# Performance work log

Measured on AMD Instinct MI355X. Metric: run time of the kernel, lower is better.

## Reference

```python
import jax, jax.numpy as jnp
import numpy as np

N_ELEC, N_NUC, D, F, E = 1024, 256, 64, 64, 131072
HH, HG = 128, 128
# labels: en (elec->nuc), ne (nuc->elec), same (elec->elec), anti (elec->elec)
SRC_N = [N_ELEC, N_NUC, N_ELEC, N_ELEC]
TGT_N = [N_NUC, N_ELEC, N_ELEC, N_ELEC]


def setup_inputs() -> dict:
    key = jax.random.key(0)
    ks = jax.random.split(key, 16)
    s_elec = jax.random.normal(ks[0], (N_ELEC, D), jnp.float32)
    v_elec = jax.random.normal(ks[1], (N_ELEC, D, 3), jnp.float32)
    s_nuc = jax.random.normal(ks[2], (N_NUC, D), jnp.float32)
    v_nuc = jax.random.normal(ks[3], (N_NUC, D, 3), jnp.float32)
    senders = jnp.stack([jax.random.randint(jax.random.fold_in(ks[4], i), (E,), 0, SRC_N[i]) for i in range(4)]).astype(jnp.int32)
    receivers = jnp.stack([jax.random.randint(jax.random.fold_in(ks[5], i), (E,), 0, TGT_N[i]) for i in range(4)]).astype(jnp.int32)
    dist = jax.random.uniform(ks[6], (4, E, F), jnp.float32)
    dirs = jax.random.normal(ks[7], (4, E, 3), jnp.float32)
    dirs = dirs / jnp.linalg.norm(dirs, axis=-1, keepdims=True)  # unit directions
    def w_init(k, shape):
        return jax.random.normal(k, shape, jnp.float32) / jnp.sqrt(jnp.float32(shape[-2]))
    return {
        's_elec': s_elec, 'v_elec': v_elec, 's_nuc': s_nuc, 'v_nuc': v_nuc,
        'dist': dist, 'dirs': dirs,
        'W_w': w_init(ks[8], (4, F, 3 * D)),
        'W_h1': w_init(ks[9], (4, D, HH)), 'W_h2': w_init(ks[10], (4, HH, 3 * D)),
        'W_g1': w_init(ks[11], (4, 2 * D, HG)), 'W_g2': w_init(ks[12], (4, HG, 3 * D)),
        'W_V': jnp.broadcast_to(jnp.eye(D, dtype=jnp.float32), (4, D, D)),
        'W_U': jnp.broadcast_to(jnp.eye(D, dtype=jnp.float32), (4, D, D)),
        'senders': senders, 'receivers': receivers,
    }


def _painn_layer(s_elec, v_elec, s_nuc, v_nuc, dist, dirs, W_w, W_h1, W_h2, W_g1, W_g2, W_V, W_U, senders, receivers):
    src_s = [s_elec, s_nuc, s_elec, s_elec]
    src_v = [v_elec, v_nuc, v_elec, v_elec]
    ds_e = jnp.zeros_like(s_elec); dv_e = jnp.zeros_like(v_elec)
    ds_n = jnp.zeros_like(s_nuc); dv_n = jnp.zeros_like(v_nuc)
    for i in range(4):
        n_tgt = TGT_N[i]
        # edge MLPs: w (1-layer, last linear) and h (2-layer silu, last linear), bias-free
        we = dist[i] @ W_w[i]                                   # [E, 3D]
        h_all = jax.nn.silu(src_s[i] @ W_h1[i]) @ W_h2[i]        # [n_src, 3D]
        hx = h_all[senders[i]]                                   # gather per edge
        phi_s, phi_vv, phi_vs = jnp.split(we * hx, 3, axis=-1)   # each [E, D]
        z_s = jax.ops.segment_sum(phi_s, receivers[i], n_tgt)    # [n_tgt, D]
        vv = phi_vv[..., None] * src_v[i][senders[i]]            # [E, D, 3]
        vs = phi_vs[..., None] * dirs[i][:, None, :]             # [E, D, 3]
        z_v = jax.ops.segment_sum(vv + vs, receivers[i], n_tgt)  # [n_tgt, D, 3]
        Vv = jnp.einsum('ndi,df->nfi', z_v, W_V[i])
        Uv = jnp.einsum('ndi,df->nfi', z_v, W_U[i])
        g_in = jnp.concatenate([z_s, (Vv ** 2).sum(axis=-1)], axis=-1)  # [n_tgt, 2D]
        gs = jax.nn.silu(g_in @ W_g1[i]) @ W_g2[i]               # [n_tgt, 3D]
        a_ss, a_vv, a_sv = jnp.split(gs, 3, axis=-1)
        upd_v = Uv * a_vv[..., None]
        upd_s = a_sv * jnp.einsum('nfi,nfi->nf', Uv, Vv) + a_ss
        if i == 0:  # 'en' -> nuclei
            ds_n = ds_n + upd_s; dv_n = dv_n + upd_v
        else:       # 'ne','same','anti' -> electrons
            ds_e = ds_e + upd_s; dv_e = dv_e + upd_v
    s_e = s_elec + ds_e
    v_e = v_elec + dv_e
    return jnp.concatenate([s_e, v_e.reshape(N_ELEC, -1)], axis=-1)


def reference(s_elec, v_elec, s_nuc, v_nuc, dist, dirs, W_w, W_h1, W_h2, W_g1, W_g2, W_V, W_U, senders, receivers):
    return _painn_layer(s_elec, v_elec, s_nuc, v_nuc, dist, dirs, W_w, W_h1, W_h2, W_g1, W_g2, W_V, W_U, senders, receivers)
```

## Files before the change

kernel.cpp:

```cpp
#include <hip/hip_runtime.h>
#include <stdint.h>

#define E_EDGES 131072
#define NELEC 1024
#define NNUC 256
#define MAXCHUNK 256
#define NBLK 16
#define UNPB 4

typedef unsigned short ushort_t;
typedef __attribute__((ext_vector_type(8))) short short8;
typedef __attribute__((ext_vector_type(4))) short short4_t;
typedef __attribute__((ext_vector_type(4))) float float4_t;
typedef __attribute__((ext_vector_type(4))) int int4_t;
typedef __attribute__((ext_vector_type(2))) unsigned int uint2_t;

__device__ inline float silu_f(float x){ return x / (1.0f + expf(-x)); }

__device__ inline short f2bf_rne(float x){
    union { float f; uint32_t u; } a; a.f = x;
    return (short)((a.u + 0x7fffu + ((a.u >> 16) & 1u)) >> 16);
}
__device__ inline float bf2f(short h){
    union { uint32_t u; float f; } a; a.u = ((uint32_t)(uint16_t)h) << 16;
    return a.f;
}
__device__ inline ushort_t bfu(float x){ return (ushort_t)f2bf_rne(x); }
__device__ inline float asf_lo(uint32_t u){ union { uint32_t u; float f; } a; a.u = u << 16; return a.f; }
__device__ inline float asf_hi(uint32_t u){ union { uint32_t u; float f; } a; a.u = u & 0xFFFF0000u; return a.f; }

__global__ __launch_bounds__(256) void prep_kernel(
    const float* __restrict__ s_elec, const float* __restrict__ v_elec,
    const float* __restrict__ s_nuc,  const float* __restrict__ v_nuc,
    const float* __restrict__ W_h1, const float* __restrict__ W_h2,
    const float* __restrict__ W_w,
    const int* __restrict__ receivers,
    ushort_t* __restrict__ tabA, ushort_t* __restrict__ tabB,
    short* __restrict__ fragH, short* __restrict__ fragL,
    int* __restrict__ bh, float* __restrict__ out)
{
    int b = blockIdx.x, tid = threadIdx.x;
    __shared__ float sls[8][64];
    __shared__ float hidls[128][8];
    __shared__ int hist[1024];

    if (b < 288){
        int t, node0;
        if (b < 32){ t = 0; node0 = b*8; }
        else if (b < 160){ t = 1; node0 = (b-32)*8; }
        else { t = 2; node0 = (b-160)*8; }
        int tp = t + 1;
        const float* src = (t == 0) ? s_nuc : s_elec;
        const float* vsrc = (t == 0) ? v_nuc : v_elec;
        long baseA = (t == 0) ? 0 : (t == 1 ? 32768 : 163840);
        long baseB = (t == 0) ? 0 : (t == 1 ? 65536 : 327680);
        for (int i = tid; i < 512; i += 256){ int n = i >> 6, f = i & 63; sls[n][f] = src[(node0+n)*64 + f]; }
        __syncthreads();
        {
            int j = tid & 127, nh = tid >> 7;
            const float* w1 = W_h1 + (long)tp*64*128;
            float a0=0,a1=0,a2=0,a3=0;
            #pragma unroll 8
            for (int f = 0; f < 64; f++){
                float w = w1[f*128 + j];
                a0 += sls[nh*4+0][f]*w; a1 += sls[nh*4+1][f]*w;
                a2 += sls[nh*4+2][f]*w; a3 += sls[nh*4+3][f]*w;
            }
            float4_t hv = { silu_f(a0), silu_f(a1), silu_f(a2), silu_f(a3) };
            *(float4_t*)&hidls[j][nh*4] = hv;
        }
        __syncthreads();
        if (tid < 192){
            const float* w2 = W_h2 + (long)tp*128*192;
            float acc[8] = {0,0,0,0,0,0,0,0};
            #pragma unroll 4
            for (int h = 0; h < 128; h++){
                float w = w2[h*192 + tid];
                float4_t ha = *(float4_t*)&hidls[h][0];
                float4_t hb = *(float4_t*)&hidls[h][4];
                acc[0]+=ha[0]*w; acc[1]+=ha[1]*w; acc[2]+=ha[2]*w; acc[3]+=ha[3]*w;
                acc[4]+=hb[0]*w; acc[5]+=hb[1]*w; acc[6]+=hb[2]*w; acc[7]+=hb[3]*w;
            }
            int p = tid >> 6, d2 = tid & 63;
            if (p == 0){
                #pragma unroll
                for (int n = 0; n < 8; n++)
                    tabA[baseA + (long)((node0+n)*64 + d2)*2 + 0] = bfu(acc[n]);
            } else if (p == 2){
                #pragma unroll
                for (int n = 0; n < 8; n++)
                    tabA[baseA + (long)((node0+n)*64 + d2)*2 + 1] = bfu(acc[n]);
            } else {
                #pragma unroll
                for (int n = 0; n < 8; n++){
                    const float* vp = vsrc + (long)(node0+n)*192 + d2*3;
                    long o = baseB + (long)((node0+n)*64 + d2)*4;
                    tabB[o+0] = bfu(acc[n]*vp[0]);
                    tabB[o+1] = bfu(acc[n]*vp[1]);
                    tabB[o+2] = bfu(acc[n]*vp[2]);
                }
            }
        }
    } else if (b < 291){
        int t = b - 288, tp = t + 1;
        const float* W = W_w + (long)tp*64*192;
        for (int idx = tid; idx < 12288; idx += 256){
            int j    = idx & 7;
            int lane = (idx >> 3) & 63;
            int ks   = (idx >> 9) & 1;
            int nt   = idx >> 10;
            int k = ks*32 + ((lane >> 4) & 3)*8 + j;
            int n = nt*16 + (lane & 15);
            float v = W[k*192 + n];
            short hi = f2bf_rne(v);
            short lo = f2bf_rne(v - bf2f(hi));
            fragH[t*12288 + idx] = hi;
            fragL[t*12288 + idx] = lo;
        }
    } else if (b < 547){
        int i = (b - 291)*256 + tid;
        int n = i >> 6, c4 = i & 63;
        float4_t v;
        if (c4 < 16) v = *(const float4_t*)(s_elec + n*64 + c4*4);
        else         v = *(const float4_t*)(v_elec + n*192 + (c4-16)*4);
        *(float4_t*)(out + n*256 + c4*4) = v;
    } else {
        int hb = b - 547, t = hb >> 4, blk = hb & 15;
        for (int i = tid; i < 1024; i += 256) hist[i] = 0;
        __syncthreads();
        long base = (long)(t+1)*E_EDGES + blk*8192;
        #pragma unroll 4
        for (int it = 0; it < 32; it++){
            int r = receivers[base + it*256 + tid];
            atomicAdd(&hist[r], 1);
        }
        __syncthreads();
        for (int bin = tid; bin < 1024; bin += 256)
            bh[(t*1024 + bin)*NBLK + blk] = hist[bin];
    }
}

__global__ __launch_bounds__(1024) void scan_kernel(int* __restrict__ bh,
                                                    int* __restrict__ offs,
                                                    int* __restrict__ counts){
    __shared__ int buf[1024];
    int t = blockIdx.x;
    int tid = threadIdx.x;
    int base = (t*1024 + tid)*NBLK;
    int vals[NBLK];
    const int4_t* p = (const int4_t*)(bh + base);
    int s = 0;
    #pragma unroll
    for (int j = 0; j < NBLK/4; j++){
        int4_t x = p[j];
        vals[j*4+0]=x[0]; vals[j*4+1]=x[1]; vals[j*4+2]=x[2]; vals[j*4+3]=x[3];
        s += x[0]+x[1]+x[2]+x[3];
    }
    buf[tid] = s;
    __syncthreads();
    int x = s;
    for (int off = 1; off < 1024; off <<= 1){
        int y = (tid >= off) ? buf[tid - off] : 0;
        __syncthreads();
        x += y; buf[tid] = x;
        __syncthreads();
    }
    int run = t*E_EDGES + (x - s);
    offs[t*1024 + tid] = run;
    counts[t*1024 + tid] = s;
    #pragma unroll
    for (int j = 0; j < NBLK; j++){
        bh[base + j] = run;
        run += vals[j];
    }
}

__global__ __launch_bounds__(256) void scatter_kernel(const int* __restrict__ receivers,
                                                      const int* __restrict__ senders,
                                                      const int* __restrict__ bh,
                                                      int* __restrict__ sorted){
    int hb = blockIdx.x, t = hb >> 4, blk = hb & 15;
    int tid = threadIdx.x;
    __shared__ int cur[1024];
    for (int bin = tid; bin < 1024; bin += 256) cur[bin] = bh[(t*1024 + bin)*NBLK + blk];
    __syncthreads();
    long base = (long)(t+1)*E_EDGES + blk*8192;
    #pragma unroll 2
    for (int it = 0; it < 32; it++){
        int e = blk*8192 + it*256 + tid;
        int r = receivers[base + it*256 + tid];
        int snd = senders[base + it*256 + tid];
        int pos = atomicAdd(&cur[r], 1);
        sorted[pos] = e | (snd << 17);
    }
}

__global__ __launch_bounds__(256) void edge_kernel(
    const float* __restrict__ dist, const float* __restrict__ dirs,
    const ushort_t* __restrict__ tabA, const ushort_t* __restrict__ tabB,
    const short* __restrict__ fragH, const short* __restrict__ fragL,
    const int* __restrict__ counts, const int* __restrict__ offs, const int* __restrict__ sorted,
    float* __restrict__ zbuf)
{
    int b = blockIdx.x;
    int t = b >> 10, node = b & 1023, tp = t + 1;
    const ushort_t* ta = tabA + ((t == 0) ? 0 : (t == 1 ? 32768 : 163840));
    const ushort_t* tb = tabB + ((t == 0) ? 0 : (t == 1 ? 65536 : 327680));
    const float* dbase = dist + (long)tp*E_EDGES*64;
    const float* dirbase = dirs + (long)tp*E_EDGES*3;

    int tid = threadIdx.x;
    int w = tid >> 6, l = tid & 63;
    int q = l >> 4, c16 = l & 15;
    int d = w*16 + c16;

    __shared__ short AH[2][2][64][8];
    __shared__ short AL[2][2][64][8];
    __shared__ float dls[2][16][3];
    __shared__ int eid[MAXCHUNK];
    __shared__ int sid[MAXCHUNK];

    short8 bhf[3][2], blf[3][2];
    #pragma unroll
    for (int ni = 0; ni < 3; ni++){
        int nt = w + ni*4;
        #pragma unroll
        for (int ks = 0; ks < 2; ks++){
            long base = (long)t*12288 + ((nt*2 + ks)*64 + l)*8;
            bhf[ni][ks] = *(const short8*)(fragH + base);
            blf[ni][ks] = *(const short8*)(fragL + base);
        }
    }

    float acc_s = 0.f, acc_v0 = 0.f, acc_v1 = 0.f, acc_v2 = 0.f;

    int deg   = counts[t*1024 + node];
    int start = offs[t*1024 + node];

    int m = tid >> 4, seg = tid & 15;
    int ks_w = seg >> 3, quad_w = (seg >> 1) & 3, j0_w = (seg & 1)*4;
    int lane2 = m | (quad_w << 4);
    int mm = tid / 3, ii = tid - mm*3;

    const float4_t z4 = {0.f,0.f,0.f,0.f};

    for (int cbase = 0; cbase < deg; cbase += MAXCHUNK){
        int chunk = deg - cbase; if (chunk > MAXCHUNK) chunk = MAXCHUNK;
        __syncthreads();
        {
            int v = 0;
            if (tid < chunk) v = sorted[(long)start + cbase + tid];
            eid[tid] = v & 131071;
            sid[tid] = ((unsigned)v) >> 17;
        }
        __syncthreads();

        int ngroups = (chunk + 15) >> 4;
        float4_t dv = z4;
        if (m < chunk) dv = *(const float4_t*)(dbase + (long)eid[m]*64 + seg*4);
        float dirv = 0.f;
        if (tid < 48 && mm < chunk) dirv = dirbase[(long)eid[mm]*3 + ii];
        uint32_t gA[4]; uint2_t gB[4];
        #pragma unroll
        for (int r = 0; r < 4; r++){
            int s = sid[q*4 + r];
            gA[r] = *(const uint32_t*)(ta + (long)(s*64 + d)*2);
            gB[r] = *(const uint2_t*)(tb + (long)(s*64 + d)*4);
        }

        for (int g = 0; g < ngroups; g++){
            int buf = g & 1;
            {
                short4_t h4, l4;
                #pragma unroll
                for (int jj = 0; jj < 4; jj++){
                    short hi = f2bf_rne(dv[jj]);
                    h4[jj] = hi;
                    l4[jj] = f2bf_rne(dv[jj] - bf2f(hi));
                }
                *(short4_t*)&AH[buf][ks_w][lane2][j0_w] = h4;
                *(short4_t*)&AL[buf][ks_w][lane2][j0_w] = l4;
                if (tid < 48) dls[buf][mm][ii] = dirv;
            }
            float4_t dvn = z4; float dirn = 0.f;
            uint32_t gAn[4] = {0,0,0,0}; uint2_t gBn[4] = {{0,0},{0,0},{0,0},{0,0}};
            if (g + 1 < ngroups){
                int li = (g+1)*16 + m;
                if (li < chunk) dvn = *(const float4_t*)(dbase + (long)eid[li]*64 + seg*4);
                int li2 = (g+1)*16 + mm;
                if (tid < 48 && li2 < chunk) dirn = dirbase[(long)eid[li2]*3 + ii];
                #pragma unroll
                for (int r = 0; r < 4; r++){
                    int s = sid[(g+1)*16 + q*4 + r];
                    gAn[r] = *(const uint32_t*)(ta + (long)(s*64 + d)*2);
                    gBn[r] = *(const uint2_t*)(tb + (long)(s*64 + d)*4);
                }
            }
            __syncthreads();

            short8 ah0 = *(short8*)&AH[buf][0][l][0];
            short8 ah1 = *(short8*)&AH[buf][1][l][0];
            short8 al0 = *(short8*)&AL[buf][0][l][0];
            short8 al1 = *(short8*)&AL[buf][1][l][0];
            float4_t C[3];
            #pragma unroll
            for (int ni = 0; ni < 3; ni++){
                float4_t acc = z4;
                acc = __builtin_amdgcn_mfma_f32_16x16x32_bf16(ah0, bhf[ni][0], acc, 0, 0, 0);
                acc = __builtin_amdgcn_mfma_f32_16x16x32_bf16(ah1, bhf[ni][1], acc, 0, 0, 0);
                acc = __builtin_amdgcn_mfma_f32_16x16x32_bf16(ah0, blf[ni][0], acc, 0, 0, 0);
                acc = __builtin_amdgcn_mfma_f32_16x16x32_bf16(ah1, blf[ni][1], acc, 0, 0, 0);
                acc = __builtin_amdgcn_mfma_f32_16x16x32_bf16(al0, bhf[ni][0], acc, 0, 0, 0);
                acc = __builtin_amdgcn_mfma_f32_16x16x32_bf16(al1, bhf[ni][1], acc, 0, 0, 0);
                C[ni] = acc;
            }

            #pragma unroll
            for (int r = 0; r < 4; r++){
                int mr = q*4 + r;
                float hs  = asf_lo(gA[r]);
                float hvs = asf_hi(gA[r]);
                float hv0 = asf_lo(gB[r][0]);
                float hv1 = asf_hi(gB[r][0]);
                float hv2 = asf_lo(gB[r][1]);
                acc_s += C[0][r] * hs;
                float pvs = C[2][r] * hvs;
                acc_v0 += C[1][r]*hv0 + pvs * dls[buf][mr][0];
                acc_v1 += C[1][r]*hv1 + pvs * dls[buf][mr][1];
                acc_v2 += C[1][r]*hv2 + pvs * dls[buf][mr][2];
            }
            dv = dvn; dirv = dirn;
            #pragma unroll
            for (int r = 0; r < 4; r++){ gA[r] = gAn[r]; gB[r] = gBn[r]; }
        }
    }

    acc_s  += __shfl_xor(acc_s, 16);  acc_s  += __shfl_xor(acc_s, 32);
    acc_v0 += __shfl_xor(acc_v0, 16); acc_v0 += __shfl_xor(acc_v0, 32);
    acc_v1 += __shfl_xor(acc_v1, 16); acc_v1 += __shfl_xor(acc_v1, 32);
    acc_v2 += __shfl_xor(acc_v2, 16); acc_v2 += __shfl_xor(acc_v2, 32);
    if (l < 16){
        float* zp = zbuf + ((long)(t*1024 + node))*256;
        zp[d] = acc_s;
        zp[64 + d*3 + 0] = acc_v0;
        zp[64 + d*3 + 1] = acc_v1;
        zp[64 + d*3 + 2] = acc_v2;
    }
}

__global__ __launch_bounds__(256) void update_kernel(
    const float* __restrict__ W_V, const float* __restrict__ W_U,
    const float* __restrict__ W_g1, const float* __restrict__ W_g2,
    const float* __restrict__ zbuf, float* __restrict__ out)
{
    int b = blockIdx.x;
    int t = b >> 8, tp = t + 1;
    int nb = (b & 255) * UNPB;
    int tid = threadIdx.x;

    __shared__ float zls[UNPB][256];
    __shared__ float Vv[UNPB][64][3], Uv[UNPB][64][3];
    __shared__ float gin[UNPB][128];
    __shared__ float hid[UNPB][128];
    __shared__ float aL[UNPB][192];
    __shared__ float vdot[UNPB][64];

    {
        int n = tid >> 6, c = tid & 63;
        *(float4_t*)&zls[n][c*4] =
            *(const float4_t*)(zbuf + ((long)(t*1024 + nb + n))*256 + c*4);
    }
    __syncthreads();

    {
        int f = tid & 63, n = tid >> 6;
        const float* wv = W_V + (long)tp*4096;
        const float* wu = W_U + (long)tp*4096;
        float av0=0,av1=0,av2=0,au0=0,au1=0,au2=0;
        #pragma unroll 4
        for (int dd = 0; dd < 64; dd++){
            float wvv = wv[dd*64 + f], wuu = wu[dd*64 + f];
            float z0 = zls[n][64 + dd*3 + 0];
            float z1 = zls[n][64 + dd*3 + 1];
            float z2 = zls[n][64 + dd*3 + 2];
            av0 += z0*wvv; av1 += z1*wvv; av2 += z2*wvv;
            au0 += z0*wuu; au1 += z1*wuu; au2 += z2*wuu;
        }
        Vv[n][f][0]=av0; Vv[n][f][1]=av1; Vv[n][f][2]=av2;
        Uv[n][f][0]=au0; Uv[n][f][1]=au1; Uv[n][f][2]=au2;
    }
    __syncthreads();

    {
        int n = tid >> 6, f = tid & 63;
        float v0=Vv[n][f][0], v1=Vv[n][f][1], v2=Vv[n][f][2];
        float u0=Uv[n][f][0], u1=Uv[n][f][1], u2=Uv[n][f][2];
        gin[n][f]      = zls[n][f];
        gin[n][64 + f] = v0*v0 + v1*v1 + v2*v2;
        vdot[n][f]     = u0*v0 + u1*v1 + u2*v2;
    }
    __syncthreads();

    {
        int h = tid & 127, ng = tid >> 7;
        const float* w1 = W_g1 + (long)tp*16384;
        float a0=0, a1=0;
        #pragma unroll 4
        for (int c = 0; c < 128; c++){
            float w = w1[c*128 + h];
            a0 += gin[ng*2+0][c]*w;
            a1 += gin[ng*2+1][c]*w;
        }
        hid[ng*2+0][h] = silu_f(a0);
        hid[ng*2+1][h] = silu_f(a1);
    }
    __syncthreads();

    if (tid < 192){
        const float* w2 = W_g2 + (long)tp*24576;
        float a0=0,a1=0,a2=0,a3=0;
        #pragma unroll 4
        for (int h = 0; h < 128; h++){
            float w = w2[h*192 + tid];
            a0 += hid[0][h]*w; a1 += hid[1][h]*w;
            a2 += hid[2][h]*w; a3 += hid[3][h]*w;
        }
        aL[0][tid]=a0; aL[1][tid]=a1; aL[2][tid]=a2; aL[3][tid]=a3;
    }
    __syncthreads();

    {
        int n = tid >> 6, f = tid & 63;
        float upd = aL[n][128 + f]*vdot[n][f] + aL[n][f];
        atomicAdd(&out[(nb + n)*256 + f], upd);
        float g = aL[n][64 + f];
        #pragma unroll
        for (int i = 0; i < 3; i++){
            float updv = Uv[n][f][i] * g;
            atomicAdd(&out[(nb + n)*256 + 64 + f*3 + i], updv);
        }
    }
}

__global__ __launch_bounds__(256) void main_kernel(
    const float* __restrict__ dist, const float* __restrict__ dirs,
    const float* __restrict__ W_V, const float* __restrict__ W_U,
    const float* __restrict__ W_g1, const float* __restrict__ W_g2,
    const ushort_t* __restrict__ tabA, const ushort_t* __restrict__ tabB,
    const short* __restrict__ fragH, const short* __restrict__ fragL,
    const int* __restrict__ counts, const int* __restrict__ offs, const int* __restrict__ sorted,
    float* __restrict__ out)
{
    int b = blockIdx.x;
    int t = b >> 10, node = b & 1023, tp = t + 1;
    const ushort_t* ta = tabA + ((t == 0) ? 0 : (t == 1 ? 32768 : 163840));
    const ushort_t* tb = tabB + ((t == 0) ? 0 : (t == 1 ? 65536 : 327680));
    const float* dbase = dist + (long)tp*E_EDGES*64;
    const float* dirbase = dirs + (long)tp*E_EDGES*3;

    int tid = threadIdx.x;
    int w = tid >> 6, l = tid & 63;
    int q = l >> 4, c16 = l & 15;
    int d = w*16 + c16;

    __shared__ short AH[2][2][64][8];
    __shared__ short AL[2][2][64][8];
    __shared__ float dls[2][16][3];
    __shared__ int eid[MAXCHUNK];
    __shared__ int sid[MAXCHUNK];
    __shared__ float zs[64];
    __shared__ float zv[64][3];
    __shared__ float VvL[192], UvL[192];
    __shared__ float gin[128], hidl[128], aLrr[192], vdotL[64];

    short8 bhf[3][2], blf[3][2];
    #pragma unroll
    for (int ni = 0; ni < 3; ni++){
        int nt = w + ni*4;
        #pragma unroll
        for (int ks = 0; ks < 2; ks++){
            long base = (long)t*12288 + ((nt*2 + ks)*64 + l)*8;
            bhf[ni][ks] = *(const short8*)(fragH + base);
            blf[ni][ks] = *(const short8*)(fragL + base);
        }
    }

    float acc_s = 0.f, acc_v0 = 0.f, acc_v1 = 0.f, acc_v2 = 0.f;

    int deg   = counts[t*1024 + node];
    int start = offs[t*1024 + node];

    int m = tid >> 4, seg = tid & 15;
    int ks_w = seg >> 3, quad_w = (seg >> 1) & 3, j0_w = (seg & 1)*4;
    int lane2 = m | (quad_w << 4);
    int mm = tid / 3, ii = tid - mm*3;

    const float4_t z4 = {0.f,0.f,0.f,0.f};

    for (int cbase = 0; cbase < deg; cbase += MAXCHUNK){
        int chunk = deg - cbase; if (chunk > MAXCHUNK) chunk = MAXCHUNK;
        __syncthreads();
        {
            int v = 0;
            if (tid < chunk) v = sorted[(long)start + cbase + tid];
            eid[tid] = v & 131071;
            sid[tid] = ((unsigned)v) >> 17;
        }
        __syncthreads();

        int ngroups = (chunk + 15) >> 4;
        float4_t dv = z4;
        if (m < chunk) dv = *(const float4_t*)(dbase + (long)eid[m]*64 + seg*4);
        float dirv = 0.f;
        if (tid < 48 && mm < chunk) dirv = dirbase[(long)eid[mm]*3 + ii];
        uint32_t gA[4]; uint2_t gB[4];
        #pragma unroll
        for (int r = 0; r < 4; r++){
            int s = sid[q*4 + r];
            gA[r] = *(const uint32_t*)(ta + (long)(s*64 + d)*2);
            gB[r] = *(const uint2_t*)(tb + (long)(s*64 + d)*4);
        }

        for (int g = 0; g < ngroups; g++){
            int buf = g & 1;
            {
                short4_t h4, l4;
                #pragma unroll
                for (int jj = 0; jj < 4; jj++){
                    short hi = f2bf_rne(dv[jj]);
                    h4[jj] = hi;
                    l4[jj] = f2bf_rne(dv[jj] - bf2f(hi));
                }
                *(short4_t*)&AH[buf][ks_w][lane2][j0_w] = h4;
                *(short4_t*)&AL[buf][ks_w][lane2][j0_w] = l4;
                if (tid < 48) dls[buf][mm][ii] = dirv;
            }
            float4_t dvn = z4; float dirn = 0.f;
            uint32_t gAn[4] = {0,0,0,0}; uint2_t gBn[4] = {{0,0},{0,0},{0,0},{0,0}};
            if (g + 1 < ngroups){
                int li = (g+1)*16 + m;
                if (li < chunk) dvn = *(const float4_t*)(dbase + (long)eid[li]*64 + seg*4);
                int li2 = (g+1)*16 + mm;
                if (tid < 48 && li2 < chunk) dirn = dirbase[(long)eid[li2]*3 + ii];
                #pragma unroll
                for (int r = 0; r < 4; r++){
                    int s = sid[(g+1)*16 + q*4 + r];
                    gAn[r] = *(const uint32_t*)(ta + (long)(s*64 + d)*2);
                    gBn[r] = *(const uint2_t*)(tb + (long)(s*64 + d)*4);
                }
            }
            __syncthreads();

            short8 ah0 = *(short8*)&AH[buf][0][l][0];
            short8 ah1 = *(short8*)&AH[buf][1][l][0];
            short8 al0 = *(short8*)&AL[buf][0][l][0];
            short8 al1 = *(short8*)&AL[buf][1][l][0];
            float4_t C[3];
            #pragma unroll
            for (int ni = 0; ni < 3; ni++){
                float4_t acc = z4;
                acc = __builtin_amdgcn_mfma_f32_16x16x32_bf16(ah0, bhf[ni][0], acc, 0, 0, 0);
                acc = __builtin_amdgcn_mfma_f32_16x16x32_bf16(ah1, bhf[ni][1], acc, 0, 0, 0);
                acc = __builtin_amdgcn_mfma_f32_16x16x32_bf16(ah0, blf[ni][0], acc, 0, 0, 0);
                acc = __builtin_amdgcn_mfma_f32_16x16x32_bf16(ah1, blf[ni][1], acc, 0, 0, 0);
                acc = __builtin_amdgcn_mfma_f32_16x16x32_bf16(al0, bhf[ni][0], acc, 0, 0, 0);
                acc = __builtin_amdgcn_mfma_f32_16x16x32_bf16(al1, bhf[ni][1], acc, 0, 0, 0);
                C[ni] = acc;
            }

            #pragma unroll
            for (int r = 0; r < 4; r++){
                int mr = q*4 + r;
                float hs  = asf_lo(gA[r]);
                float hvs = asf_hi(gA[r]);
                float hv0 = asf_lo(gB[r][0]);
                float hv1 = asf_hi(gB[r][0]);
                float hv2 = asf_lo(gB[r][1]);
                acc_s += C[0][r] * hs;
                float pvs = C[2][r] * hvs;
                acc_v0 += C[1][r]*hv0 + pvs * dls[buf][mr][0];
                acc_v1 += C[1][r]*hv1 + pvs * dls[buf][mr][1];
                acc_v2 += C[1][r]*hv2 + pvs * dls[buf][mr][2];
            }
            dv = dvn; dirv = dirn;
            #pragma unroll
            for (int r = 0; r < 4; r++){ gA[r] = gAn[r]; gB[r] = gBn[r]; }
        }
    }

    acc_s  += __shfl_xor(acc_s, 16);  acc_s  += __shfl_xor(acc_s, 32);
    acc_v0 += __shfl_xor(acc_v0, 16); acc_v0 += __shfl_xor(acc_v0, 32);
    acc_v1 += __shfl_xor(acc_v1, 16); acc_v1 += __shfl_xor(acc_v1, 32);
    acc_v2 += __shfl_xor(acc_v2, 16); acc_v2 += __shfl_xor(acc_v2, 32);
    __syncthreads();
    if (l < 16){
        zs[d] = acc_s;
        zv[d][0] = acc_v0; zv[d][1] = acc_v1; zv[d][2] = acc_v2;
    }
    __syncthreads();

    if (tid < 192){
        int i = tid >> 6, f = tid & 63;
        const float* wv = W_V + (long)tp*64*64;
        const float* wu = W_U + (long)tp*64*64;
        float av = 0.f, au = 0.f;
        #pragma unroll 8
        for (int dd = 0; dd < 64; dd++){
            float z = zv[dd][i];
            av += z * wv[dd*64 + f];
            au += z * wu[dd*64 + f];
        }
        VvL[f*3 + i] = av;
        UvL[f*3 + i] = au;
    }
    __syncthreads();
    if (tid < 64){
        int f = tid;
        float v0 = VvL[f*3], v1 = VvL[f*3+1], v2 = VvL[f*3+2];
        float u0 = UvL[f*3], u1 = UvL[f*3+1], u2 = UvL[f*3+2];
        gin[f] = zs[f];
        gin[64 + f] = v0*v0 + v1*v1 + v2*v2;
        vdotL[f] = u0*v0 + u1*v1 + u2*v2;
    }
    __syncthreads();
    if (tid < 128){
        const float* w1 = W_g1 + (long)tp*128*128;
        float acc = 0.f;
        #pragma unroll 8
        for (int c = 0; c < 128; c++) acc += gin[c] * w1[c*128 + tid];
        hidl[tid] = silu_f(acc);
    }
    __syncthreads();
    if (tid < 192){
        const float* w2 = W_g2 + (long)tp*128*192;
        float acc = 0.f;
        #pragma unroll 8
        for (int h = 0; h < 128; h++) acc += hidl[h] * w2[h*192 + tid];
        aLrr[tid] = acc;
    }
    __syncthreads();
    if (tid < 64){
        int f = tid;
        float upd = aLrr[128 + f] * vdotL[f] + aLrr[f];
        atomicAdd(&out[node*256 + f], upd);
    }
    if (tid < 192){
        int i = tid >> 6, f = tid & 63;
        float updv = UvL[f*3 + i] * aLrr[64 + f];
        atomicAdd(&out[node*256 + 64 + f*3 + i], updv);
    }
}

extern "C" void kernel_launch(void* const* d_in, const int* in_sizes, int n_in,
                              void* d_out, int out_size, void* d_ws, size_t ws_size,
                              hipStream_t stream){
    const float* s_elec  = (const float*)d_in[0];
    const float* v_elec  = (const float*)d_in[1];
    const float* s_nuc   = (const float*)d_in[2];
    const float* v_nuc   = (const float*)d_in[3];
    const float* dist    = (const float*)d_in[4];
    const float* dirs    = (const float*)d_in[5];
    const float* W_w     = (const float*)d_in[6];
    const float* W_h1    = (const float*)d_in[7];
    const float* W_h2    = (const float*)d_in[8];
    const float* W_g1    = (const float*)d_in[9];
    const float* W_g2    = (const float*)d_in[10];
    const float* W_V     = (const float*)d_in[11];
    const float* W_U     = (const float*)d_in[12];
    const int* senders   = (const int*)d_in[13];
    const int* receivers = (const int*)d_in[14];
    float* out = (float*)d_out;
    char* ws = (char*)d_ws;

    ushort_t* tabA  = (ushort_t*)(ws + 0);
    ushort_t* tabB  = (ushort_t*)(ws + 589824);
    short* fragH  = (short*)(ws + 1769472);
    short* fragL  = (short*)(ws + 1843200);
    int*   bh     = (int*)  (ws + 1916928);
    int*   offs   = (int*)  (ws + 2113536);
    int*   counts = (int*)  (ws + 2125824);
    int*   sorted = (int*)  (ws + 2138112);
    float* zbuf   = (float*)(ws + 3710976);
    if (ws_size < 3710976) return;
    bool split = (ws_size >= 6856704);

    prep_kernel<<<dim3(595), dim3(256), 0, stream>>>(
        s_elec, v_elec, s_nuc, v_nuc, W_h1, W_h2, W_w, receivers,
        tabA, tabB, fragH, fragL, bh, out);
    scan_kernel<<<dim3(3), dim3(1024), 0, stream>>>(bh, offs, counts);
    scatter_kernel<<<dim3(48), dim3(256), 0, stream>>>(receivers, senders, bh, sorted);
    if (split){
        edge_kernel<<<dim3(3072), dim3(256), 0, stream>>>(
            dist, dirs, tabA, tabB, fragH, fragL, counts, offs, sorted, zbuf);
        update_kernel<<<dim3(768), dim3(256), 0, stream>>>(
            W_V, W_U, W_g1, W_g2, zbuf, out);
    } else {
        main_kernel<<<dim3(3072), dim3(256), 0, stream>>>(
            dist, dirs, W_V, W_U, W_g1, W_g2,
            tabA, tabB, fragH, fragL, counts, offs, sorted, out);
    }
}
```

Measured before the change: 339.4 us.

## Stage whole edge chunk of dist into swizzled LDS before MFMA loop

The edge kernel now loads and splits the dist rows for up to 128 edges at once into XOR-swizzled shared memory, with two threads per edge each doing 32-byte loads, instead of double-buffering 16 edges per group with one barrier per group. The inner group loop then has no barriers and reads MFMA fragments straight from LDS, while the per-group table gathers are issued just in time rather than prefetched. This is meant to raise memory-level parallelism and remove per-group synchronisation. In exchange it uses more LDS per block and gives up the overlap of table gathers with compute.

Result: no change. 344.9 us (+1.6%).

```diff
diff --git a/kernel.cpp b/kernel.cpp
--- a/kernel.cpp
+++ b/kernel.cpp
@@ -5,6 +5,7 @@
 #define NELEC 1024
 #define NNUC 256
 #define MAXCHUNK 256
+#define ECHUNK 128
 #define NBLK 16
 #define UNPB 4
 
@@ -12,6 +13,7 @@
 typedef __attribute__((ext_vector_type(8))) short short8;
 typedef __attribute__((ext_vector_type(4))) short short4_t;
 typedef __attribute__((ext_vector_type(4))) float float4_t;
+typedef __attribute__((ext_vector_type(8))) float float8_t;
 typedef __attribute__((ext_vector_type(4))) int int4_t;
 typedef __attribute__((ext_vector_type(2))) unsigned int uint2_t;
 
@@ -203,22 +205,22 @@
     float* __restrict__ zbuf)
 {
     int b = blockIdx.x;
-    int t = b >> 10, node = b & 1023, tp = t + 1;
+    int t = b >> 10, node = b & 1023;
     const ushort_t* ta = tabA + ((t == 0) ? 0 : (t == 1 ? 32768 : 163840));
     const ushort_t* tb = tabB + ((t == 0) ? 0 : (t == 1 ? 65536 : 327680));
-    const float* dbase = dist + (long)tp*E_EDGES*64;
-    const float* dirbase = dirs + (long)tp*E_EDGES*3;
+    const float* dbase = dist + (long)(t+1)*E_EDGES*64;
+    const float* dirbase = dirs + (long)(t+1)*E_EDGES*3;
 
     int tid = threadIdx.x;
     int w = tid >> 6, l = tid & 63;
     int q = l >> 4, c16 = l & 15;
     int d = w*16 + c16;
-
-    __shared__ short AH[2][2][64][8];
-    __shared__ short AL[2][2][64][8];
-    __shared__ float dls[2][16][3];
-    __shared__ int eid[MAXCHUNK];
-    __shared__ int sid[MAXCHUNK];
+    int se = tid >> 1, sk = tid & 1;
+
+    __shared__ short AHs[ECHUNK*64];
+    __shared__ short ALs[ECHUNK*64];
+    __shared__ int sid[ECHUNK];
+    __shared__ float dls[ECHUNK][3];
 
     short8 bhf[3][2], blf[3][2];
     #pragma unroll
@@ -237,71 +239,64 @@
     int deg   = counts[t*1024 + node];
     int start = offs[t*1024 + node];
 
-    int m = tid >> 4, seg = tid & 15;
-    int ks_w = seg >> 3, quad_w = (seg >> 1) & 3, j0_w = (seg & 1)*4;
-    int lane2 = m | (quad_w << 4);
-    int mm = tid / 3, ii = tid - mm*3;
-
     const float4_t z4 = {0.f,0.f,0.f,0.f};
-
-    for (int cbase = 0; cbase < deg; cbase += MAXCHUNK){
-        int chunk = deg - cbase; if (chunk > MAXCHUNK) chunk = MAXCHUNK;
-        __syncthreads();
+    const float8_t z8 = {0.f,0.f,0.f,0.f,0.f,0.f,0.f,0.f};
+
+    for (int cbase = 0; cbase < deg; cbase += ECHUNK){
+        int chunk = deg - cbase; if (chunk > ECHUNK) chunk = ECHUNK;
+        __syncthreads();
+
+        bool okA = (se < chunk);
+        int vA = okA ? sorted[(long)start + cbase + se] : 0;
+        if (tid < ECHUNK){
+            int v = (tid < chunk) ? sorted[(long)start + cbase + tid] : 0;
+            sid[tid] = ((unsigned)v) >> 17;
+            float d0=0.f, d1=0.f, d2=0.f;
+            if (tid < chunk){
+                const float* dp = dirbase + (long)(v & 131071)*3;
+                d0 = dp[0]; d1 = dp[1]; d2 = dp[2];
+            }
+            dls[tid][0]=d0; dls[tid][1]=d1; dls[tid][2]=d2;
+        }
         {
-            int v = 0;
-            if (tid < chunk) v = sorted[(long)start + cbase + tid];
-            eid[tid] = v & 131071;
-            sid[tid] = ((unsigned)v) >> 17;
+            long ebase = okA ? ((long)(vA & 131071)*64 + sk*32) : 0;
+            #pragma unroll
+            for (int j = 0; j < 4; j++){
+                float8_t f = z8;
+                if (okA) f = *(const float8_t*)(dbase + ebase + j*8);
+                short8 h8, l8;
+                #pragma unroll
+                for (int jj = 0; jj < 8; jj++){
+                    short hi = f2bf_rne(f[jj]);
+                    h8[jj] = hi;
+                    l8[jj] = f2bf_rne(f[jj] - bf2f(hi));
+                }
+                int slot = (sk*4 + j) ^ (se & 7);
+                *(short8*)&AHs[se*64 + slot*8] = h8;
+                *(short8*)&ALs[se*64 + slot*8] = l8;
+            }
         }
         __syncthreads();
 
         int ngroups = (chunk + 15) >> 4;
-        float4_t dv = z4;
-        if (m < chunk) dv = *(const float4_t*)(dbase + (long)eid[m]*64 + seg*4);
-        float dirv = 0.f;
-        if (tid < 48 && mm < chunk) dirv = dirbase[(long)eid[mm]*3 + ii];
-        uint32_t gA[4]; uint2_t gB[4];
-        #pragma unroll
-        for (int r = 0; r < 4; r++){
-            int s = sid[q*4 + r];
-            gA[r] = *(const uint32_t*)(ta + (long)(s*64 + d)*2);
-            gB[r] = *(const uint2_t*)(tb + (long)(s*64 + d)*4);
-        }
-
         for (int g = 0; g < ngroups; g++){
-            int buf = g & 1;
-            {
-                short4_t h4, l4;
-                #pragma unroll
-                for (int jj = 0; jj < 4; jj++){
-                    short hi = f2bf_rne(dv[jj]);
-                    h4[jj] = hi;
-                    l4[jj] = f2bf_rne(dv[jj] - bf2f(hi));
-                }
-                *(short4_t*)&AH[buf][ks_w][lane2][j0_w] = h4;
-                *(short4_t*)&AL[buf][ks_w][lane2][j0_w] = l4;
-                if (tid < 48) dls[buf][mm][ii] = dirv;
-            }
-            float4_t dvn = z4; float dirn = 0.f;
-            uint32_t gAn[4] = {0,0,0,0}; uint2_t gBn[4] = {{0,0},{0,0},{0,0},{0,0}};
-            if (g + 1 < ngroups){
-                int li = (g+1)*16 + m;
-                if (li < chunk) dvn = *(const float4_t*)(dbase + (long)eid[li]*64 + seg*4);
-                int li2 = (g+1)*16 + mm;
-                if (tid < 48 && li2 < chunk) dirn = dirbase[(long)eid[li2]*3 + ii];
-                #pragma unroll
-                for (int r = 0; r < 4; r++){
-                    int s = sid[(g+1)*16 + q*4 + r];
-                    gAn[r] = *(const uint32_t*)(ta + (long)(s*64 + d)*2);
-                    gBn[r] = *(const uint2_t*)(tb + (long)(s*64 + d)*4);
-                }
-            }
-            __syncthreads();
-
-            short8 ah0 = *(short8*)&AH[buf][0][l][0];
-            short8 ah1 = *(short8*)&AH[buf][1][l][0];
-            short8 al0 = *(short8*)&AL[buf][0][l][0];
-            short8 al1 = *(short8*)&AL[buf][1][l][0];
+            int mrb = g*16 + q*4;
+            uint32_t gA[4]; uint2_t gB[4];
+            #pragma unroll
+            for (int r = 0; r < 4; r++){
+                int s = sid[mrb + r];
+                gA[r] = *(const uint32_t*)(ta + (long)(s*64 + d)*2);
+                gB[r] = *(const uint2_t*)(tb + (long)(s*64 + d)*4);
+            }
+            int e  = g*16 + c16;
+            int sw = e & 7;
+            int o0 = e*64 + ((q ^ sw) * 8);
+            int o1 = e*64 + (((4 + q) ^ sw) * 8);
+            short8 ah0 = *(short8*)&AHs[o0];
+            short8 ah1 = *(short8*)&AHs[o1];
+            short8 al0 = *(short8*)&ALs[o0];
+            short8 al1 = *(short8*)&ALs[o1];
+
             float4_t C[3];
             #pragma unroll
             for (int ni = 0; ni < 3; ni++){
@@ -317,7 +312,7 @@
 
             #pragma unroll
             for (int r = 0; r < 4; r++){
-                int mr = q*4 + r;
+                int mr = mrb + r;
                 float hs  = asf_lo(gA[r]);
                 float hvs = asf_hi(gA[r]);
                 float hv0 = asf_lo(gB[r][0]);
@@ -325,13 +320,10 @@
                 float hv2 = asf_lo(gB[r][1]);
                 acc_s += C[0][r] * hs;
                 float pvs = C[2][r] * hvs;
-                acc_v0 += C[1][r]*hv0 + pvs * dls[buf][mr][0];
-                acc_v1 += C[1][r]*hv1 + pvs * dls[buf][mr][1];
-                acc_v2 += C[1][r]*hv2 + pvs * dls[buf][mr][2];
-            }
-            dv = dvn; dirv = dirn;
-            #pragma unroll
-            for (int r = 0; r < 4; r++){ gA[r] = gAn[r]; gB[r] = gBn[r]; }
+                acc_v0 += C[1][r]*hv0 + pvs * dls[mr][0];
+                acc_v1 += C[1][r]*hv1 + pvs * dls[mr][1];
+                acc_v2 += C[1][r]*hv2 + pvs * dls[mr][2];
+            }
         }
     }
 
```

## Stage 32-edge supergroups with 8-float loads, packed bf16 convert, swizzled LDS

Applied to the files above, without the earlier changes.

The edge kernel now stages 32 edges per barrier instead of 16. Each thread loads 8 contiguous floats of the dist row, converts them with the packed v_cvt_pk_bf16_f32 instruction into hi/lo bf16 splits, and writes them to an XOR-swizzled LDS row layout. Two 16-edge MFMA groups then run per staged buffer, which halves the number of __syncthreads, widens global loads and avoids LDS bank conflicts. The sender-table gather prefetch moves into the inner group loop. The risks are a different rounding path from the hardware convert and higher register pressure.

Result: no change. 333.1 us (median of 2 runs) (-1.9%).

```diff
diff --git a/kernel.cpp b/kernel.cpp
--- a/kernel.cpp
+++ b/kernel.cpp
@@ -12,6 +12,7 @@
 typedef __attribute__((ext_vector_type(8))) short short8;
 typedef __attribute__((ext_vector_type(4))) short short4_t;
 typedef __attribute__((ext_vector_type(4))) float float4_t;
+typedef __attribute__((ext_vector_type(8))) float float8_t;
 typedef __attribute__((ext_vector_type(4))) int int4_t;
 typedef __attribute__((ext_vector_type(2))) unsigned int uint2_t;
 
@@ -203,20 +204,22 @@
     float* __restrict__ zbuf)
 {
     int b = blockIdx.x;
-    int t = b >> 10, node = b & 1023, tp = t + 1;
+    int t = b >> 10, node = b & 1023;
     const ushort_t* ta = tabA + ((t == 0) ? 0 : (t == 1 ? 32768 : 163840));
     const ushort_t* tb = tabB + ((t == 0) ? 0 : (t == 1 ? 65536 : 327680));
-    const float* dbase = dist + (long)tp*E_EDGES*64;
-    const float* dirbase = dirs + (long)tp*E_EDGES*3;
+    const float* dbase = dist + (long)(t+1)*E_EDGES*64;
+    const float* dirbase = dirs + (long)(t+1)*E_EDGES*3;
 
     int tid = threadIdx.x;
     int w = tid >> 6, l = tid & 63;
     int q = l >> 4, c16 = l & 15;
     int d = w*16 + c16;
-
-    __shared__ short AH[2][2][64][8];
-    __shared__ short AL[2][2][64][8];
-    __shared__ float dls[2][16][3];
+    int srow = tid >> 3, seg8 = tid & 7;
+    int mm = tid / 3, ii = tid - mm*3;
+
+    __shared__ __attribute__((aligned(16))) short AHs[2][2048];
+    __shared__ __attribute__((aligned(16))) short ALs[2][2048];
+    __shared__ float dls[2][32][3];
     __shared__ int eid[MAXCHUNK];
     __shared__ int sid[MAXCHUNK];
 
@@ -237,12 +240,8 @@
     int deg   = counts[t*1024 + node];
     int start = offs[t*1024 + node];
 
-    int m = tid >> 4, seg = tid & 15;
-    int ks_w = seg >> 3, quad_w = (seg >> 1) & 3, j0_w = (seg & 1)*4;
-    int lane2 = m | (quad_w << 4);
-    int mm = tid / 3, ii = tid - mm*3;
-
     const float4_t z4 = {0.f,0.f,0.f,0.f};
+    const float8_t z8 = {0.f,0.f,0.f,0.f,0.f,0.f,0.f,0.f};
 
     for (int cbase = 0; cbase < deg; cbase += MAXCHUNK){
         int chunk = deg - cbase; if (chunk > MAXCHUNK) chunk = MAXCHUNK;
@@ -255,11 +254,12 @@
         }
         __syncthreads();
 
+        int nsg = (chunk + 31) >> 5;
         int ngroups = (chunk + 15) >> 4;
-        float4_t dv = z4;
-        if (m < chunk) dv = *(const float4_t*)(dbase + (long)eid[m]*64 + seg*4);
-        float dirv = 0.f;
-        if (tid < 48 && mm < chunk) dirv = dirbase[(long)eid[mm]*3 + ii];
+
+        float8_t f8 = z8; float dirv = 0.f;
+        if (srow < chunk) f8 = *(const float8_t*)(dbase + (long)eid[srow]*64 + seg8*8);
+        if (tid < 96 && mm < chunk) dirv = dirbase[(long)eid[mm]*3 + ii];
         uint32_t gA[4]; uint2_t gB[4];
         #pragma unroll
         for (int r = 0; r < 4; r++){
@@ -268,70 +268,89 @@
             gB[r] = *(const uint2_t*)(tb + (long)(s*64 + d)*4);
         }
 
-        for (int g = 0; g < ngroups; g++){
-            int buf = g & 1;
+        for (int sg = 0; sg < nsg; sg++){
+            int buf = sg & 1;
             {
-                short4_t h4, l4;
-                #pragma unroll
-                for (int jj = 0; jj < 4; jj++){
-                    short hi = f2bf_rne(dv[jj]);
-                    h4[jj] = hi;
-                    l4[jj] = f2bf_rne(dv[jj] - bf2f(hi));
+                union { int4_t i; short8 s; } H, L;
+                #pragma unroll
+                for (int p = 0; p < 4; p++){
+                    float a0 = f8[2*p], a1 = f8[2*p+1];
+                    uint32_t hp, lp;
+                    asm("v_cvt_pk_bf16_f32 %0, %1, %2" : "=v"(hp) : "v"(a0), "v"(a1));
+                    float r0 = asf_lo(hp), r1 = asf_hi(hp);
+                    asm("v_cvt_pk_bf16_f32 %0, %1, %2" : "=v"(lp) : "v"(a0 - r0), "v"(a1 - r1));
+                    H.i[p] = (int)hp; L.i[p] = (int)lp;
                 }
-                *(short4_t*)&AH[buf][ks_w][lane2][j0_w] = h4;
-                *(short4_t*)&AL[buf][ks_w][lane2][j0_w] = l4;
-                if (tid < 48) dls[buf][mm][ii] = dirv;
-            }
-            float4_t dvn = z4; float dirn = 0.f;
-            uint32_t gAn[4] = {0,0,0,0}; uint2_t gBn[4] = {{0,0},{0,0},{0,0},{0,0}};
-            if (g + 1 < ngroups){
-                int li = (g+1)*16 + m;
-                if (li < chunk) dvn = *(const float4_t*)(dbase + (long)eid[li]*64 + seg*4);
-                int li2 = (g+1)*16 + mm;
-                if (tid < 48 && li2 < chunk) dirn = dirbase[(long)eid[li2]*3 + ii];
+                int o = srow*64 + ((seg8 ^ (srow & 7))*8);
+                *(short8*)&AHs[buf][o] = H.s;
+                *(short8*)&ALs[buf][o] = L.s;
+                if (tid < 96) dls[buf][mm][ii] = dirv;
+            }
+            float8_t f8n = z8; float dirn = 0.f;
+            {
+                int nb = (sg + 1)*32;
+                if (nb < chunk){
+                    int ri = nb + srow;
+                    if (ri < chunk) f8n = *(const float8_t*)(dbase + (long)eid[ri]*64 + seg8*8);
+                    int ri2 = nb + mm;
+                    if (tid < 96 && ri2 < chunk) dirn = dirbase[(long)eid[ri2]*3 + ii];
+                }
+            }
+            __syncthreads();
+
+            int gmax = ngroups - sg*2; if (gmax > 2) gmax = 2;
+            for (int g2 = 0; g2 < gmax; g2++){
+                int gg = sg*2 + g2;
+                uint32_t gAn[4] = {0,0,0,0};
+                uint2_t  gBn[4] = {{0,0},{0,0},{0,0},{0,0}};
+                if (gg + 1 < ngroups){
+                    int mrb2 = (gg+1)*16 + q*4;
+                    #pragma unroll
+                    for (int r = 0; r < 4; r++){
+                        int s = sid[mrb2 + r];
+                        gAn[r] = *(const uint32_t*)(ta + (long)(s*64 + d)*2);
+                        gBn[r] = *(const uint2_t*)(tb + (long)(s*64 + d)*4);
+                    }
+                }
+                int ro = g2*16 + c16;
+                int sw = ro & 7;
+                short8 ah0 = *(short8*)&AHs[buf][ro*64 + ((q ^ sw)*8)];
+                short8 ah1 = *(short8*)&AHs[buf][ro*64 + (((4 + q) ^ sw)*8)];
+                short8 al0 = *(short8*)&ALs[buf][ro*64 + ((q ^ sw)*8)];
+                short8 al1 = *(short8*)&ALs[buf][ro*64 + (((4 + q) ^ sw)*8)];
+
+                float4_t C[3];
+                #pragma unroll
+                for (int ni = 0; ni < 3; ni++){
+                    float4_t acc = z4;
+                    acc = __builtin_amdgcn_mfma_f32_16x16x32_bf16(ah0, bhf[ni][0], acc, 0, 0, 0);
+                    acc = __builtin_amdgcn_mfma_f32_16x16x32_bf16(ah1, bhf[ni][1], acc, 0, 0, 0);
+                    acc = __builtin_amdgcn_mfma_f32_16x16x32_bf16(ah0, blf[ni][0], acc, 0, 0, 0);
+                    acc = __builtin_amdgcn_mfma_f32_16x16x32_bf16(ah1, blf[ni][1], acc, 0, 0, 0);
+                    acc = __builtin_amdgcn_mfma_f32_16x16x32_bf16(al0, bhf[ni][0], acc, 0, 0, 0);
+                    acc = __builtin_amdgcn_mfma_f32_16x16x32_bf16(al1, bhf[ni][1], acc, 0, 0, 0);
+                    C[ni] = acc;
+                }
+
+                int mrb = g2*16 + q*4;
                 #pragma unroll
                 for (int r = 0; r < 4; r++){
-                    int s = sid[(g+1)*16 + q*4 + r];
-                    gAn[r] = *(const uint32_t*)(ta + (long)(s*64 + d)*2);
-                    gBn[r] = *(const uint2_t*)(tb + (long)(s*64 + d)*4);
+                    int mr = mrb + r;
+                    float hs  = asf_lo(gA[r]);
+                    float hvs = asf_hi(gA[r]);
+                    float hv0 = asf_lo(gB[r][0]);
+                    float hv1 = asf_hi(gB[r][0]);
+                    float hv2 = asf_lo(gB[r][1]);
+                    acc_s += C[0][r] * hs;
+                    float pvs = C[2][r] * hvs;
+                    acc_v0 += C[1][r]*hv0 + pvs * dls[buf][mr][0];
+                    acc_v1 += C[1][r]*hv1 + pvs * dls[buf][mr][1];
+                    acc_v2 += C[1][r]*hv2 + pvs * dls[buf][mr][2];
                 }
-            }
-            __syncthreads();
-
-            short8 ah0 = *(short8*)&AH[buf][0][l][0];
-            short8 ah1 = *(short8*)&AH[buf][1][l][0];
-            short8 al0 = *(short8*)&AL[buf][0][l][0];
-            short8 al1 = *(short8*)&AL[buf][1][l][0];
-            float4_t C[3];
-            #pragma unroll
-            for (int ni = 0; ni < 3; ni++){
-                float4_t acc = z4;
-                acc = __builtin_amdgcn_mfma_f32_16x16x32_bf16(ah0, bhf[ni][0], acc, 0, 0, 0);
-                acc = __builtin_amdgcn_mfma_f32_16x16x32_bf16(ah1, bhf[ni][1], acc, 0, 0, 0);
-                acc = __builtin_amdgcn_mfma_f32_16x16x32_bf16(ah0, blf[ni][0], acc, 0, 0, 0);
-                acc = __builtin_amdgcn_mfma_f32_16x16x32_bf16(ah1, blf[ni][1], acc, 0, 0, 0);
-                acc = __builtin_amdgcn_mfma_f32_16x16x32_bf16(al0, bhf[ni][0], acc, 0, 0, 0);
-                acc = __builtin_amdgcn_mfma_f32_16x16x32_bf16(al1, bhf[ni][1], acc, 0, 0, 0);
-                C[ni] = acc;
-            }
-
-            #pragma unroll
-            for (int r = 0; r < 4; r++){
-                int mr = q*4 + r;
-                float hs  = asf_lo(gA[r]);
-                float hvs = asf_hi(gA[r]);
-                float hv0 = asf_lo(gB[r][0]);
-                float hv1 = asf_hi(gB[r][0]);
-                float hv2 = asf_lo(gB[r][1]);
-                acc_s += C[0][r] * hs;
-                float pvs = C[2][r] * hvs;
-                acc_v0 += C[1][r]*hv0 + pvs * dls[buf][mr][0];
-                acc_v1 += C[1][r]*hv1 + pvs * dls[buf][mr][1];
-                acc_v2 += C[1][r]*hv2 + pvs * dls[buf][mr][2];
-            }
-            dv = dvn; dirv = dirn;
-            #pragma unroll
-            for (int r = 0; r < 4; r++){ gA[r] = gAn[r]; gB[r] = gBn[r]; }
+                #pragma unroll
+                for (int r = 0; r < 4; r++){ gA[r] = gAn[r]; gB[r] = gBn[r]; }
+            }
+            f8 = f8n; dirv = dirn;
         }
     }
 
```
